# Performance work log

Hardware: AMD Instinct MI355X
Metric: run time of the kernel (lower is better)

Reference implementation:

```python
import jax, jax.numpy as jnp
import numpy as np

N_USERS = 100000
N_TIRES = 100000
N_BRANDS = 100
N_SIZES = 500
HGT = 128
SPEC = 64
TEXT = 384
TPROJ = 64
HID = 128
OUT = 64
T_EVENTS = 2000000


def _lin_init(key, fan_in, fan_out):
    kw, kb = jax.random.split(key)
    s = 1.0 / np.sqrt(fan_in)
    W = jax.random.uniform(kw, (fan_in, fan_out), jnp.float32, -s, s)
    b = jax.random.uniform(kb, (fan_out,), jnp.float32, -s, s)
    return W, b


def setup_inputs() -> dict:
    key = jax.random.key(0)
    ks = jax.random.split(key, 18)
    inp = {
        "h_user": jax.random.normal(ks[0], (N_USERS, HGT), jnp.float32),
        "h_tire": jax.random.normal(ks[1], (N_TIRES, HGT), jnp.float32),
        "h_brand": jax.random.normal(ks[2], (N_BRANDS, HGT), jnp.float32),
        "h_size": jax.random.normal(ks[3], (N_SIZES, HGT), jnp.float32),
        "tire_specs": jax.random.normal(ks[4], (N_TIRES, SPEC), jnp.float32),
        "text_emb": jax.random.normal(ks[5], (N_TIRES, TEXT), jnp.float32),
        "tire_brand_idx": jax.random.randint(ks[6], (N_TIRES,), 0, N_BRANDS, jnp.int32),
        "tire_size_idx": jax.random.randint(ks[7], (N_TIRES,), 0, N_SIZES, jnp.int32),
        "hist_items": jax.random.randint(ks[8], (T_EVENTS,), 0, N_TIRES, jnp.int32),
        "hist_segments": jnp.sort(jax.random.randint(ks[9], (T_EVENTS,), 0, N_USERS, jnp.int32)),
    }
    # text projection
    inp["W_tp"], inp["b_tp"] = _lin_init(ks[10], TEXT, TPROJ)
    # item tower MLP: in = 3*HGT + SPEC + TPROJ = 512
    item_in = 3 * HGT + SPEC + TPROJ
    inp["W_i1"], inp["b_i1"] = _lin_init(ks[11], item_in, HID)
    inp["W_i2"], inp["b_i2"] = _lin_init(ks[12], HID, HID)
    inp["W_i3"], inp["b_i3"] = _lin_init(ks[13], HID, OUT)
    # user tower MLP: in = HGT + OUT = 192
    user_in = HGT + OUT
    inp["W_u1"], inp["b_u1"] = _lin_init(ks[14], user_in, HID)
    inp["W_u2"], inp["b_u2"] = _lin_init(ks[15], HID, HID)
    inp["W_u3"], inp["b_u3"] = _lin_init(ks[16], HID, OUT)
    return inp


def _mlp(x, W1, b1, W2, b2, W3, b3):
    h = jax.nn.relu(x @ W1 + b1)
    h = jax.nn.relu(h @ W2 + b2)
    return h @ W3 + b3


def _l2norm(x):
    n = jnp.sqrt(jnp.sum(x * x, axis=-1, keepdims=True))
    return x / jnp.maximum(n, 1e-12)


def reference(h_user, h_tire, h_brand, h_size, tire_specs, text_emb,
              tire_brand_idx, tire_size_idx, hist_items, hist_segments,
              W_tp, b_tp, W_i1, b_i1, W_i2, b_i2, W_i3, b_i3,
              W_u1, b_u1, W_u2, b_u2, W_u3, b_u3):
    n_users = h_user.shape[0]
    # item tower (dropout = identity in eval)
    text_proj = jax.nn.relu(text_emb @ W_tp + b_tp)  # [T, 64]
    x_item = jnp.concatenate(
        [h_tire, h_brand[tire_brand_idx], h_size[tire_size_idx], tire_specs, text_proj],
        axis=-1)  # [T, 512]
    item_vec = _l2norm(_mlp(x_item, W_i1, b_i1, W_i2, b_i2, W_i3, b_i3))  # [T, 64]
    # ragged history mean-pool as one segment-mean pass
    gathered = item_vec[hist_items]  # [E, 64]
    sums = jax.ops.segment_sum(gathered, hist_segments, num_segments=n_users)
    counts = jax.ops.segment_sum(jnp.ones((hist_items.shape[0],), item_vec.dtype),
                                 hist_segments, num_segments=n_users)[:, None]
    history_pool = jnp.where(counts > 0, sums / jnp.maximum(counts, 1.0), 0.0)
    # user tower
    x_user = jnp.concatenate([h_user, history_pool], axis=-1)  # [U, 192]
    user_vec = _l2norm(_mlp(x_user, W_u1, b_u1, W_u2, b_u2, W_u3, b_u3))  # [U, 64]
    return user_vec, item_vec
```

## Files before the change

### kernel.cpp

```cpp
#include <hip/hip_runtime.h>

typedef __bf16 bf16;
typedef __bf16 bf16x4 __attribute__((ext_vector_type(4)));
typedef __bf16 bf16x8 __attribute__((ext_vector_type(8)));
typedef float f32x4 __attribute__((ext_vector_type(4)));

__device__ inline float bfbits(unsigned u) { return __builtin_bit_cast(float, u); }

__device__ inline bf16x8 cvt8p(f32x4 x0, f32x4 x1) {
  bf16x8 a;
  a[0] = (bf16)x0[0]; a[1] = (bf16)x0[1]; a[2] = (bf16)x0[2]; a[3] = (bf16)x0[3];
  a[4] = (bf16)x1[0]; a[5] = (bf16)x1[1]; a[6] = (bf16)x1[2]; a[7] = (bf16)x1[3];
  return a;
}

#define MFMA16(a, b, c) __builtin_amdgcn_mfma_f32_16x16x32_bf16((a), (b), (c), 0, 0, 0)

__device__ inline void gload16(const void* g, void* l) {
  __builtin_amdgcn_global_load_lds(
      (const __attribute__((address_space(1))) void*)g,
      (__attribute__((address_space(3))) void*)l, 16, 0, 0);
}

#define BARRIER()                      \
  do {                                 \
    asm volatile("" ::: "memory");     \
    __builtin_amdgcn_s_barrier();      \
    asm volatile("" ::: "memory");     \
  } while (0)

template <int N>
__device__ inline void waitcnt_vm() {
  asm volatile("s_waitcnt vmcnt(%0)" ::"i"(N) : "memory");
}

struct WEnt { const float* src; bf16* dst; int K; int N; int mode; int base; };
struct WprepArgs { WEnt e[9]; int nent; int total; float* zb; };

__global__ __launch_bounds__(256) void wprep_all(WprepArgs a) {
  int idx = blockIdx.x * 256 + threadIdx.x;
  if (idx < 128) a.zb[idx] = 0.0f;
  if (idx >= a.total) return;
  int ei = 0;
  while (ei + 1 < a.nent && idx >= a.e[ei + 1].base) ++ei;
  const WEnt E = a.e[ei];
  int li = idx - E.base;
  int lane = li & 63, fi = li >> 6;
  int NT = E.N / 16;
  int kt = fi / NT, nt = fi % NT;
  int krow = kt * 32 + ((lane >> 4) << 3);
  int col = nt * 16 + (lane & 15);
  bf16* d = E.dst + (size_t)li * 8;
#pragma unroll
  for (int j = 0; j < 8; ++j) {
    int r = krow + j;
    if (E.mode == 1) r = (r < 128) ? r : r + 256;
    d[j] = (bf16)E.src[(size_t)r * E.N + col];
  }
}

__global__ __launch_bounds__(256) void seg_bounds(const int* __restrict__ hsegs,
                                                  int* __restrict__ bound, int E, int U) {
  int e = blockIdx.x * 256 + threadIdx.x;
  if (e > E) return;
  if (e == 0) {
    int b = hsegs[0];
    for (int u = 0; u <= b; ++u) bound[u] = 0;
  } else if (e == E) {
    int a = hsegs[E - 1];
    for (int u = a + 1; u <= U; ++u) bound[u] = E;
  } else {
    int a = hsegs[e - 1], b = hsegs[e];
    for (int u = a + 1; u <= b; ++u) bound[u] = e;
  }
}

struct GemmArgs {
  const void* a0; const bf16* wfrag; const float* bias; void* out; int M;
};

template <int K, int N, int NW>
__global__ __launch_bounds__(NW * 64) void gemm_k(GemmArgs g) {
  constexpr int KT = K / 32, NT = N / 16;
  constexpr int TROWS = NW * 32;
  __shared__ bf16 wlds[K * N];
  {
    const uint4* s = (const uint4*)g.wfrag;
    uint4* d = (uint4*)wlds;
    constexpr int CH = K * N * 2 / 16;
    for (int i = threadIdx.x; i < CH; i += NW * 64) d[i] = s[i];
  }
  __syncthreads();

  const int lane = threadIdx.x & 63;
  const int wave = threadIdx.x >> 6;
  const int kgo = (lane >> 4) << 3;
  const int ntiles = (g.M + TROWS - 1) / TROWS;

  for (int tile = blockIdx.x; tile < ntiles; tile += gridDim.x) {
    const int rowbase = tile * TROWS;
    const int rw = rowbase + wave * 16 + (lane & 15);
    const int r0 = min(rw, g.M - 1);
    const int r1 = min(rw + NW * 16, g.M - 1);

    f32x4 acc[2][NT] = {};
#pragma unroll 2
    for (int kt = 0; kt < KT; ++kt) {
      const int kc = kt * 32 + kgo;
      const f32x4* q0 = (const f32x4*)((const float*)g.a0 + (size_t)r0 * K + kc);
      const f32x4* q1 = (const f32x4*)((const float*)g.a0 + (size_t)r1 * K + kc);
      bf16x8 a0 = cvt8p(q0[0], q0[1]);
      bf16x8 a1 = cvt8p(q1[0], q1[1]);
      const bf16x8* bp = ((const bf16x8*)wlds) + kt * NT * 64 + lane;
#pragma unroll
      for (int nt = 0; nt < NT; ++nt) {
        bf16x8 b = bp[nt * 64];
        acc[0][nt] = MFMA16(a0, b, acc[0][nt]);
        acc[1][nt] = MFMA16(a1, b, acc[1][nt]);
      }
    }

    const int colbase = lane & 15;
    const int rgrp = (lane >> 4) * 4;
#pragma unroll
    for (int m = 0; m < 2; ++m) {
      const int rbase = rowbase + m * (NW * 16) + wave * 16 + rgrp;
#pragma unroll
      for (int j = 0; j < 4; ++j) {
        const int r = rbase + j;
        if (r < g.M) {
#pragma unroll
          for (int nt = 0; nt < NT; ++nt) {
            float v = acc[m][nt][j] + g.bias[colbase + nt * 16];
            ((float*)g.out)[(size_t)r * N + colbase + nt * 16] = v;
          }
        }
      }
    }
  }
}

struct TpArgs { const float* text; const bf16* wf; const float* bias; bf16* out; int M; };

__global__ __launch_bounds__(256, 4) void tp_k(TpArgs g) {
  __shared__ float abuf[2][128 * 32];
  const int tid = threadIdx.x, lane = tid & 63, wave = tid >> 6;
  const int kgo = (lane >> 4) << 3, colbase = lane & 15, r4 = (lane >> 4) * 4;
  const int rowbase = blockIdx.x << 7;

  auto stage = [&](int kt, int bi) {
#pragma unroll
    for (int i = 0; i < 4; ++i) {
      const int q = i * 256 + wave * 64 + lane;
      const int row = q >> 3;
      const int c = (lane & 7) ^ (row & 7);
      const int rg = min(rowbase + row, g.M - 1);
      const float* src = g.text + (size_t)rg * 384 + kt * 32 + c * 4;
      gload16(src, (char*)abuf[bi] + (size_t)(i * 256 + wave * 64) * 16);
    }
  };

  stage(0, 0);
  f32x4 acc[2][4] = {};
  for (int kt = 0; kt < 12; ++kt) {
    if (kt + 1 < 12) {
      stage(kt + 1, (kt + 1) & 1);
      waitcnt_vm<4>();
    } else {
      waitcnt_vm<0>();
    }
    BARRIER();
    const float* buf = abuf[kt & 1];
#pragma unroll
    for (int m = 0; m < 2; ++m) {
      const int row = m * 64 + wave * 16 + colbase;
      const int c0 = kgo >> 2;
      f32x4 x0 = *(const f32x4*)(buf + row * 32 + ((c0 ^ (row & 7)) << 2));
      f32x4 x1 = *(const f32x4*)(buf + row * 32 + (((c0 + 1) ^ (row & 7)) << 2));
      bf16x8 a = cvt8p(x0, x1);
      const bf16x8* bp = ((const bf16x8*)g.wf) + kt * 4 * 64 + lane;
#pragma unroll
      for (int nt = 0; nt < 4; ++nt)
        acc[m][nt] = MFMA16(a, bp[nt * 64], acc[m][nt]);
    }
    BARRIER();
  }

#pragma unroll
  for (int m = 0; m < 2; ++m) {
    const int rbase = rowbase + m * 64 + wave * 16 + r4;
#pragma unroll
    for (int j = 0; j < 4; ++j) {
      const int r = rbase + j;
      if (r < g.M) {
#pragma unroll
        for (int nt = 0; nt < 4; ++nt) {
          float v = fmaxf(acc[m][nt][j] + g.bias[colbase + nt * 16], 0.0f);
          g.out[(size_t)r * 64 + colbase + nt * 16] = (bf16)v;
        }
      }
    }
  }
}

struct TowerArgs {
  const void* a0; const void* a1; const void* a2;
  const int* bidx; const int* sidx;
  const float* brandC; const float* sizeC;
  const bf16* wf1; const bf16* wf2; const bf16* wf3;
  const float* b1; const float* b2; const float* b3;
  float* out; bf16* out2; int M;
};

__device__ inline bf16x8 read_afrag(const bf16* hw, int lane, int kt) {
  const int row = lane & 15;
  const int c8 = (kt * 4 + (lane >> 4)) ^ (row & 7);
  return *(const bf16x8*)(hw + row * 128 + c8 * 8);
}

template <int KT1, int DEPTH, int ASRC, int BS>
__global__ __launch_bounds__(512, 2) void tower_p(TowerArgs g) {
  static_assert(KT1 % DEPTH == 0, "pipeline rotation requires DEPTH | KT1");
  constexpr int FK = (ASRC == 2) ? 6 : 4;
  __shared__ bf16 w1[KT1 * 32 * 128];
  __shared__ bf16 w2[128 * 128];
  __shared__ bf16 w3[128 * 64];
  __shared__ bf16 ht[8][16 * 128];
  {
    const int tid = threadIdx.x;
    const uint4* s1 = (const uint4*)g.wf1; uint4* d1 = (uint4*)w1;
    for (int i = tid; i < KT1 * 32 * 128 * 2 / 16; i += 512) d1[i] = s1[i];
    const uint4* s2 = (const uint4*)g.wf2; uint4* d2 = (uint4*)w2;
    for (int i = tid; i < 128 * 128 * 2 / 16; i += 512) d2[i] = s2[i];
    const uint4* s3 = (const uint4*)g.wf3; uint4* d3 = (uint4*)w3;
    for (int i = tid; i < 128 * 64 * 2 / 16; i += 512) d3[i] = s3[i];
  }
  __syncthreads();

  const int lane = threadIdx.x & 63, wave = threadIdx.x >> 6;
  const int kgo = (lane >> 4) << 3, colbase = lane & 15, r4 = (lane >> 4) * 4;
  bf16* hw = ht[wave];
  const int ntiles = (g.M + 255) >> 8;
  const int nb = gridDim.x;

  struct Ptrs { const float* tA; const float* tB; const float* sA; const float* sB;
                const bf16* pA; const bf16* pB; };
  auto mk = [&](int t) {
    Ptrs p;
    const int rA = min(t * 256 + wave * 16 + colbase, g.M - 1);
    const int rB = min(t * 256 + 128 + wave * 16 + colbase, g.M - 1);
    p.tA = (const float*)g.a0 + (size_t)rA * 128;
    p.tB = (const float*)g.a0 + (size_t)rB * 128;
    if constexpr (ASRC == 2) {
      p.sA = (const float*)g.a1 + (size_t)rA * 64;
      p.sB = (const float*)g.a1 + (size_t)rB * 64;
      p.pA = (const bf16*)g.a2 + (size_t)rA * 64;
      p.pB = (const bf16*)g.a2 + (size_t)rB * 64;
    } else {
      p.sA = nullptr; p.sB = nullptr;
      p.pA = (const bf16*)g.a1 + (size_t)rA * 64;
      p.pB = (const bf16*)g.a1 + (size_t)rB * 64;
    }
    return p;
  };

  f32x4 st[DEPTH][4];
  auto issue = [&](f32x4* s, const Ptrs& p, int kt) {
    if (kt < 4) {
      const f32x4* qa = (const f32x4*)(p.tA + kt * 32 + kgo);
      const f32x4* qb = (const f32x4*)(p.tB + kt * 32 + kgo);
      s[0] = qa[0]; s[1] = qa[1]; s[2] = qb[0]; s[3] = qb[1];
    } else if (ASRC == 2 && kt < 6) {
      const f32x4* qa = (const f32x4*)(p.sA + (kt - 4) * 32 + kgo);
      const f32x4* qb = (const f32x4*)(p.sB + (kt - 4) * 32 + kgo);
      s[0] = qa[0]; s[1] = qa[1]; s[2] = qb[0]; s[3] = qb[1];
    } else {
      const int ko = kt - FK;
      s[0] = *(const f32x4*)(p.pA + ko * 32 + kgo);
      s[2] = *(const f32x4*)(p.pB + ko * 32 + kgo);
    }
  };

  int tile = blockIdx.x;
  Ptrs P = mk(tile);
  int tn = tile + nb; if (tn >= ntiles) tn = tile;
  Ptrs Pn = mk(tn);

#pragma unroll
  for (int s = 0; s < DEPTH; ++s) issue(st[s], P, s);

  for (;;) {
    f32x4 acc1[2][8] = {};
#pragma unroll
    for (int kt = 0; kt < KT1; ++kt) {
      const int s = kt % DEPTH;
      bf16x8 a0, a1;
      if (kt < FK) {
        a0 = cvt8p(st[s][0], st[s][1]);
        a1 = cvt8p(st[s][2], st[s][3]);
      } else {
        a0 = __builtin_bit_cast(bf16x8, st[s][0]);
        a1 = __builtin_bit_cast(bf16x8, st[s][2]);
      }
      const bf16x8* bp = ((const bf16x8*)w1) + kt * 8 * 64 + lane;
#pragma unroll
      for (int nt = 0; nt < 8; ++nt) {
        bf16x8 b = bp[nt * 64];
        acc1[0][nt] = MFMA16(a0, b, acc1[0][nt]);
        acc1[1][nt] = MFMA16(a1, b, acc1[1][nt]);
      }
      if (kt + DEPTH < KT1) issue(st[s], P, kt + DEPTH);
      else issue(st[s], Pn, kt + DEPTH - KT1);
    }

    const int rowbase = tile * 256;
    f32x4 acc3[2][4] = {};
#pragma unroll
    for (int m = 0; m < 2; ++m) {
      const int rbase = rowbase + m * 128 + wave * 16 + r4;
#pragma unroll
      for (int j = 0; j < 4; ++j) {
        const int row = r4 + j;
        const float* bc = nullptr; const float* sc = nullptr;
        if constexpr (BS != 0) {
          const int rr = min(rbase + j, g.M - 1);
          bc = g.brandC + (size_t)g.bidx[rr] * 128;
          sc = g.sizeC + (size_t)g.sidx[rr] * 128;
        }
#pragma unroll
        for (int nt = 0; nt < 8; ++nt) {
          const int col = colbase + nt * 16;
          float v = acc1[m][nt][j];
          if constexpr (BS != 0) v += bc[col] + sc[col];
          else v += g.b1[col];
          const int c8 = (col >> 3) ^ (row & 7);
          hw[row * 128 + c8 * 8 + (col & 7)] = (bf16)fmaxf(v, 0.0f);
        }
      }
      f32x4 acc2[8] = {};
#pragma unroll
      for (int kt = 0; kt < 4; ++kt) {
        bf16x8 af = read_afrag(hw, lane, kt);
        const bf16x8* bp = ((const bf16x8*)w2) + kt * 8 * 64 + lane;
#pragma unroll
        for (int nt = 0; nt < 8; ++nt)
          acc2[nt] = MFMA16(af, bp[nt * 64], acc2[nt]);
      }
#pragma unroll
      for (int j = 0; j < 4; ++j) {
        const int row = r4 + j;
#pragma unroll
        for (int nt = 0; nt < 8; ++nt) {
          const int col = colbase + nt * 16;
          float v = fmaxf(acc2[nt][j] + g.b2[col], 0.0f);
          const int c8 = (col >> 3) ^ (row & 7);
          hw[row * 128 + c8 * 8 + (col & 7)] = (bf16)v;
        }
      }
#pragma unroll
      for (int kt = 0; kt < 4; ++kt) {
        bf16x8 af = read_afrag(hw, lane, kt);
        const bf16x8* bq = ((const bf16x8*)w3) + kt * 4 * 64 + lane;
#pragma unroll
        for (int nt = 0; nt < 4; ++nt)
          acc3[m][nt] = MFMA16(af, bq[nt * 64], acc3[m][nt]);
      }
    }

#pragma unroll
    for (int m = 0; m < 2; ++m) {
      const int rbase = rowbase + m * 128 + wave * 16 + r4;
#pragma unroll
      for (int j = 0; j < 4; ++j) {
        float vv[4];
        float ssq = 0.0f;
#pragma unroll
        for (int nt = 0; nt < 4; ++nt) {
          float v = acc3[m][nt][j] + g.b3[colbase + nt * 16];
          vv[nt] = v;
          ssq += v * v;
        }
        ssq += __shfl_xor(ssq, 1);
        ssq += __shfl_xor(ssq, 2);
        ssq += __shfl_xor(ssq, 4);
        ssq += __shfl_xor(ssq, 8);
        const float scale = 1.0f / fmaxf(sqrtf(ssq), 1e-12f);
        const int r = rbase + j;
        if (r < g.M) {
          float* o = g.out + (size_t)r * 64 + colbase;
#pragma unroll
          for (int nt = 0; nt < 4; ++nt) o[nt * 16] = vv[nt] * scale;
          if (g.out2) {
            bf16* o2 = g.out2 + (size_t)r * 64 + colbase;
#pragma unroll
            for (int nt = 0; nt < 4; ++nt) o2[nt * 16] = (bf16)(vv[nt] * scale);
          }
        }
      }
    }

    if (tn == tile) break;
    tile = tn; P = Pn;
    tn = tile + nb; if (tn >= ntiles) tn = tile;
    Pn = mk(tn);
  }
}

__global__ __launch_bounds__(256) void pool_k(const int* __restrict__ hitems,
                                              const int* __restrict__ bound,
                                              const bf16* __restrict__ itemb,
                                              bf16* __restrict__ pool, int U) {
  const int lane = threadIdx.x & 63;
  const int wid = blockIdx.x * 4 + (threadIdx.x >> 6);
  const int stride = gridDim.x * 4;
  const int grp = lane >> 4, li = lane & 15;
  for (int u = wid; u < U; u += stride) {
    const int s = bound[u], e = bound[u + 1];
    f32x4 s0 = {0.f, 0.f, 0.f, 0.f}, s1 = {0.f, 0.f, 0.f, 0.f};
    f32x4 s2 = {0.f, 0.f, 0.f, 0.f}, s3 = {0.f, 0.f, 0.f, 0.f};
    int i = s + grp;
    for (; i + 12 < e; i += 16) {
      int a0 = hitems[i], a1 = hitems[i + 4], a2 = hitems[i + 8], a3 = hitems[i + 12];
      uint2 r0 = *(const uint2*)(itemb + (size_t)a0 * 64 + li * 4);
      uint2 r1 = *(const uint2*)(itemb + (size_t)a1 * 64 + li * 4);
      uint2 r2 = *(const uint2*)(itemb + (size_t)a2 * 64 + li * 4);
      uint2 r3 = *(const uint2*)(itemb + (size_t)a3 * 64 + li * 4);
      s0[0] += bfbits(r0.x << 16); s0[1] += bfbits(r0.x & 0xffff0000u);
      s0[2] += bfbits(r0.y << 16); s0[3] += bfbits(r0.y & 0xffff0000u);
      s1[0] += bfbits(r1.x << 16); s1[1] += bfbits(r1.x & 0xffff0000u);
      s1[2] += bfbits(r1.y << 16); s1[3] += bfbits(r1.y & 0xffff0000u);
      s2[0] += bfbits(r2.x << 16); s2[1] += bfbits(r2.x & 0xffff0000u);
      s2[2] += bfbits(r2.y << 16); s2[3] += bfbits(r2.y & 0xffff0000u);
      s3[0] += bfbits(r3.x << 16); s3[1] += bfbits(r3.x & 0xffff0000u);
      s3[2] += bfbits(r3.y << 16); s3[3] += bfbits(r3.y & 0xffff0000u);
    }
    for (; i < e; i += 4) {
      int a0 = hitems[i];
      uint2 r0 = *(const uint2*)(itemb + (size_t)a0 * 64 + li * 4);
      s0[0] += bfbits(r0.x << 16); s0[1] += bfbits(r0.x & 0xffff0000u);
      s0[2] += bfbits(r0.y << 16); s0[3] += bfbits(r0.y & 0xffff0000u);
    }
#pragma unroll
    for (int c = 0; c < 4; ++c) s0[c] += s1[c] + s2[c] + s3[c];
#pragma unroll
    for (int c = 0; c < 4; ++c) {
      s0[c] += __shfl_xor(s0[c], 16);
      s0[c] += __shfl_xor(s0[c], 32);
    }
    const int cnt = e - s;
    const float inv = (cnt > 0) ? 1.0f / (float)cnt : 0.0f;
    if (grp == 0) {
      bf16x4 o;
      o[0] = (bf16)(s0[0] * inv); o[1] = (bf16)(s0[1] * inv);
      o[2] = (bf16)(s0[2] * inv); o[3] = (bf16)(s0[3] * inv);
      *(bf16x4*)(pool + (size_t)u * 64 + li * 4) = o;
    }
  }
}

extern "C" void kernel_launch(void* const* d_in, const int* in_sizes, int n_in,
                              void* d_out, int out_size, void* d_ws, size_t ws_size,
                              hipStream_t stream) {
  const float* h_user = (const float*)d_in[0];
  const float* h_tire = (const float*)d_in[1];
  const float* h_brand = (const float*)d_in[2];
  const float* h_size = (const float*)d_in[3];
  const float* specs = (const float*)d_in[4];
  const float* text = (const float*)d_in[5];
  const int* bidx = (const int*)d_in[6];
  const int* sidx = (const int*)d_in[7];
  const int* hitems = (const int*)d_in[8];
  const int* hsegs = (const int*)d_in[9];
  const float* W_tp = (const float*)d_in[10]; const float* b_tp = (const float*)d_in[11];
  const float* W_i1 = (const float*)d_in[12]; const float* b_i1 = (const float*)d_in[13];
  const float* W_i2 = (const float*)d_in[14]; const float* b_i2 = (const float*)d_in[15];
  const float* W_i3 = (const float*)d_in[16]; const float* b_i3 = (const float*)d_in[17];
  const float* W_u1 = (const float*)d_in[18]; const float* b_u1 = (const float*)d_in[19];
  const float* W_u2 = (const float*)d_in[20]; const float* b_u2 = (const float*)d_in[21];
  const float* W_u3 = (const float*)d_in[22]; const float* b_u3 = (const float*)d_in[23];

  const int U = in_sizes[0] / 128;
  const int T = in_sizes[4] / 64;
  const int E = in_sizes[8];

  char* ws = (char*)d_ws;
  size_t off = 0;
  auto alloc = [&](size_t bytes) -> char* {
    char* p = ws + off;
    off += (bytes + 255) & ~(size_t)255;
    return p;
  };
  bf16* wf_tp  = (bf16*)alloc(384 * 64 * 2);
  bf16* wf_i1a = (bf16*)alloc(256 * 128 * 2);
  bf16* wf_ib  = (bf16*)alloc(128 * 128 * 2);
  bf16* wf_is  = (bf16*)alloc(128 * 128 * 2);
  bf16* wf_i2  = (bf16*)alloc(128 * 128 * 2);
  bf16* wf_i3  = (bf16*)alloc(128 * 64 * 2);
  bf16* wf_u1  = (bf16*)alloc(192 * 128 * 2);
  bf16* wf_u2  = (bf16*)alloc(128 * 128 * 2);
  bf16* wf_u3  = (bf16*)alloc(128 * 64 * 2);
  float* zb    = (float*)alloc(128 * 4);
  float* brandC = (float*)alloc(100 * 128 * 4);
  float* sizeC  = (float*)alloc(500 * 128 * 4);
  bf16* tpbuf = (bf16*)alloc((size_t)T * 64 * 2);
  bf16* pool  = (bf16*)alloc((size_t)U * 64 * 2);
  bf16* itemb = (bf16*)alloc((size_t)T * 64 * 2);
  int* bound  = (int*)alloc((size_t)(U + 1) * 4);
  (void)ws_size; (void)n_in; (void)out_size;

  WprepArgs wa = {};
  auto addent = [&](int i, const float* src, bf16* dst, int K, int N, int mode, int& run) {
    wa.e[i] = {src, dst, K, N, mode, run};
    run += (K / 32) * (N / 16) * 64;
  };
  int run = 0;
  addent(0, W_tp, wf_tp, 384, 64, 0, run);
  addent(1, W_i1, wf_i1a, 256, 128, 1, run);
  addent(2, W_i1 + 128 * 128, wf_ib, 128, 128, 0, run);
  addent(3, W_i1 + 256 * 128, wf_is, 128, 128, 0, run);
  addent(4, W_i2, wf_i2, 128, 128, 0, run);
  addent(5, W_i3, wf_i3, 128, 64, 0, run);
  addent(6, W_u1, wf_u1, 192, 128, 0, run);
  addent(7, W_u2, wf_u2, 128, 128, 0, run);
  addent(8, W_u3, wf_u3, 128, 64, 0, run);
  wa.nent = 9; wa.total = run; wa.zb = zb;
  wprep_all<<<(run + 255) / 256, 256, 0, stream>>>(wa);

  seg_bounds<<<(E + 256) / 256, 256, 0, stream>>>(hsegs, bound, E, U);

  {
    GemmArgs a = {}; a.a0 = h_brand; a.wfrag = wf_ib; a.bias = b_i1; a.out = brandC; a.M = 100;
    gemm_k<128, 128, 4><<<1, 256, 0, stream>>>(a);
  }
  {
    GemmArgs a = {}; a.a0 = h_size; a.wfrag = wf_is; a.bias = zb; a.out = sizeC; a.M = 500;
    gemm_k<128, 128, 4><<<4, 256, 0, stream>>>(a);
  }
  {
    TpArgs a = {text, wf_tp, b_tp, tpbuf, T};
    tp_k<<<(T + 127) / 128, 256, 0, stream>>>(a);
  }

  float* out_user = (float*)d_out;
  float* out_item = out_user + (size_t)U * 64;

  {
    TowerArgs a = {};
    a.a0 = h_tire; a.a1 = specs; a.a2 = tpbuf;
    a.bidx = bidx; a.sidx = sidx; a.brandC = brandC; a.sizeC = sizeC;
    a.wf1 = wf_i1a; a.wf2 = wf_i2; a.wf3 = wf_i3;
    a.b1 = zb; a.b2 = b_i2; a.b3 = b_i3;
    a.out = out_item; a.out2 = itemb; a.M = T;
    const int nt = (T + 255) / 256;
    tower_p<8, 4, 2, 1><<<min(256, nt), 512, 0, stream>>>(a);
  }

  pool_k<<<(U + 3) / 4, 256, 0, stream>>>(hitems, bound, itemb, pool, U);

  {
    TowerArgs a = {};
    a.a0 = h_user; a.a1 = pool;
    a.wf1 = wf_u1; a.wf2 = wf_u2; a.wf3 = wf_u3;
    a.b1 = b_u1; a.b2 = b_u2; a.b3 = b_u3;
    a.out = out_user; a.out2 = nullptr; a.M = U;
    const int nt = (U + 255) / 256;
    tower_p<6, 2, 3, 0><<<min(256, nt), 512, 0, stream>>>(a);
  }
}
```

Measured before the change: 246.7 us.

## Replace register-pipelined persistent tower kernel with simple one-tile-per-block loop

Removes the manual multi-stage register prefetch pipeline and the persistent grid capped at 256 blocks from the tower kernels. Each block now handles one 256-row tile with direct loads inside the K loop. The aim is lower register pressure and more blocks in flight, letting the hardware hide latency. This gives up the explicit overlap of the next tile's loads with current compute.

```diff
diff --git a/kernel.cpp b/kernel.cpp
--- a/kernel.cpp
+++ b/kernel.cpp
@@ -12,6 +12,10 @@
   a[0] = (bf16)x0[0]; a[1] = (bf16)x0[1]; a[2] = (bf16)x0[2]; a[3] = (bf16)x0[3];
   a[4] = (bf16)x1[0]; a[5] = (bf16)x1[1]; a[6] = (bf16)x1[2]; a[7] = (bf16)x1[3];
   return a;
+}
+__device__ inline bf16x8 cvt8(const float* p) {
+  const f32x4* q = (const f32x4*)p;
+  return cvt8p(q[0], q[1]);
 }
 
 #define MFMA16(a, b, c) __builtin_amdgcn_mfma_f32_16x16x32_bf16((a), (b), (c), 0, 0, 0)
@@ -107,10 +111,8 @@
 #pragma unroll 2
     for (int kt = 0; kt < KT; ++kt) {
       const int kc = kt * 32 + kgo;
-      const f32x4* q0 = (const f32x4*)((const float*)g.a0 + (size_t)r0 * K + kc);
-      const f32x4* q1 = (const f32x4*)((const float*)g.a0 + (size_t)r1 * K + kc);
-      bf16x8 a0 = cvt8p(q0[0], q0[1]);
-      bf16x8 a1 = cvt8p(q1[0], q1[1]);
+      bf16x8 a0 = cvt8((const float*)g.a0 + (size_t)r0 * K + kc);
+      bf16x8 a1 = cvt8((const float*)g.a0 + (size_t)r1 * K + kc);
       const bf16x8* bp = ((const bf16x8*)wlds) + kt * NT * 64 + lane;
 #pragma unroll
       for (int nt = 0; nt < NT; ++nt) {
@@ -212,24 +214,38 @@
   float* out; bf16* out2; int M;
 };
 
+template <int ASRC>
+__device__ inline bf16x8 tower_load_a(const TowerArgs& g, int r, int kc) {
+  if constexpr (ASRC == 2) {
+    if (kc < 128) return cvt8((const float*)g.a0 + (size_t)r * 128 + kc);
+    else if (kc < 192) return cvt8((const float*)g.a1 + (size_t)r * 64 + (kc - 128));
+    else return *(const bf16x8*)((const bf16*)g.a2 + (size_t)r * 64 + (kc - 192));
+  } else {
+    if (kc < 128) return cvt8((const float*)g.a0 + (size_t)r * 128 + kc);
+    else return *(const bf16x8*)((const bf16*)g.a1 + (size_t)r * 64 + (kc - 128));
+  }
+}
+
 __device__ inline bf16x8 read_afrag(const bf16* hw, int lane, int kt) {
   const int row = lane & 15;
   const int c8 = (kt * 4 + (lane >> 4)) ^ (row & 7);
   return *(const bf16x8*)(hw + row * 128 + c8 * 8);
 }
 
-template <int KT1, int DEPTH, int ASRC, int BS>
-__global__ __launch_bounds__(512, 2) void tower_p(TowerArgs g) {
-  static_assert(KT1 % DEPTH == 0, "pipeline rotation requires DEPTH | KT1");
-  constexpr int FK = (ASRC == 2) ? 6 : 4;
-  __shared__ bf16 w1[KT1 * 32 * 128];
-  __shared__ bf16 w2[128 * 128];
-  __shared__ bf16 w3[128 * 64];
-  __shared__ bf16 ht[8][16 * 128];
+template <int K1, int ASRC, int BS>
+__global__ __launch_bounds__(512, 2) void tower_k(TowerArgs g) {
+  constexpr int KT1 = K1 / 32;
+  constexpr int NW = 8;
+  constexpr int TROWS = NW * 32;
+  __shared__ bf16 lds[K1 * 128 + 128 * 128 + 128 * 64 + NW * 16 * 128];
+  bf16* w1 = lds;
+  bf16* w2 = lds + K1 * 128;
+  bf16* w3 = w2 + 128 * 128;
+  bf16* ht = w3 + 128 * 64;
   {
     const int tid = threadIdx.x;
     const uint4* s1 = (const uint4*)g.wf1; uint4* d1 = (uint4*)w1;
-    for (int i = tid; i < KT1 * 32 * 128 * 2 / 16; i += 512) d1[i] = s1[i];
+    for (int i = tid; i < K1 * 128 * 2 / 16; i += 512) d1[i] = s1[i];
     const uint4* s2 = (const uint4*)g.wf2; uint4* d2 = (uint4*)w2;
     for (int i = tid; i < 128 * 128 * 2 / 16; i += 512) d2[i] = s2[i];
     const uint4* s3 = (const uint4*)g.wf3; uint4* d3 = (uint4*)w3;
@@ -237,71 +253,26 @@
   }
   __syncthreads();
 
-  const int lane = threadIdx.x & 63, wave = threadIdx.x >> 6;
-  const int kgo = (lane >> 4) << 3, colbase = lane & 15, r4 = (lane >> 4) * 4;
-  bf16* hw = ht[wave];
-  const int ntiles = (g.M + 255) >> 8;
-  const int nb = gridDim.x;
-
-  struct Ptrs { const float* tA; const float* tB; const float* sA; const float* sB;
-                const bf16* pA; const bf16* pB; };
-  auto mk = [&](int t) {
-    Ptrs p;
-    const int rA = min(t * 256 + wave * 16 + colbase, g.M - 1);
-    const int rB = min(t * 256 + 128 + wave * 16 + colbase, g.M - 1);
-    p.tA = (const float*)g.a0 + (size_t)rA * 128;
-    p.tB = (const float*)g.a0 + (size_t)rB * 128;
-    if constexpr (ASRC == 2) {
-      p.sA = (const float*)g.a1 + (size_t)rA * 64;
-      p.sB = (const float*)g.a1 + (size_t)rB * 64;
-      p.pA = (const bf16*)g.a2 + (size_t)rA * 64;
-      p.pB = (const bf16*)g.a2 + (size_t)rB * 64;
-    } else {
-      p.sA = nullptr; p.sB = nullptr;
-      p.pA = (const bf16*)g.a1 + (size_t)rA * 64;
-      p.pB = (const bf16*)g.a1 + (size_t)rB * 64;
-    }
-    return p;
-  };
-
-  f32x4 st[DEPTH][4];
-  auto issue = [&](f32x4* s, const Ptrs& p, int kt) {
-    if (kt < 4) {
-      const f32x4* qa = (const f32x4*)(p.tA + kt * 32 + kgo);
-      const f32x4* qb = (const f32x4*)(p.tB + kt * 32 + kgo);
-      s[0] = qa[0]; s[1] = qa[1]; s[2] = qb[0]; s[3] = qb[1];
-    } else if (ASRC == 2 && kt < 6) {
-      const f32x4* qa = (const f32x4*)(p.sA + (kt - 4) * 32 + kgo);
-      const f32x4* qb = (const f32x4*)(p.sB + (kt - 4) * 32 + kgo);
-      s[0] = qa[0]; s[1] = qa[1]; s[2] = qb[0]; s[3] = qb[1];
-    } else {
-      const int ko = kt - FK;
-      s[0] = *(const f32x4*)(p.pA + ko * 32 + kgo);
-      s[2] = *(const f32x4*)(p.pB + ko * 32 + kgo);
-    }
-  };
-
-  int tile = blockIdx.x;
-  Ptrs P = mk(tile);
-  int tn = tile + nb; if (tn >= ntiles) tn = tile;
-  Ptrs Pn = mk(tn);
-
-#pragma unroll
-  for (int s = 0; s < DEPTH; ++s) issue(st[s], P, s);
-
-  for (;;) {
+  const int lane = threadIdx.x & 63;
+  const int wave = threadIdx.x >> 6;
+  const int kgo = (lane >> 4) << 3;
+  const int colbase = lane & 15;
+  const int r4 = (lane >> 4) * 4;
+  bf16* hw = ht + wave * (16 * 128);
+  const int ntiles = (g.M + TROWS - 1) / TROWS;
+
+  for (int tile = blockIdx.x; tile < ntiles; tile += gridDim.x) {
+    const int rowbase = tile * TROWS;
+    const int rw = rowbase + wave * 16 + colbase;
+    const int r0 = min(rw, g.M - 1);
+    const int r1 = min(rw + NW * 16, g.M - 1);
+
     f32x4 acc1[2][8] = {};
-#pragma unroll
+#pragma unroll 2
     for (int kt = 0; kt < KT1; ++kt) {
-      const int s = kt % DEPTH;
-      bf16x8 a0, a1;
-      if (kt < FK) {
-        a0 = cvt8p(st[s][0], st[s][1]);
-        a1 = cvt8p(st[s][2], st[s][3]);
-      } else {
-        a0 = __builtin_bit_cast(bf16x8, st[s][0]);
-        a1 = __builtin_bit_cast(bf16x8, st[s][2]);
-      }
+      const int kc = kt * 32 + kgo;
+      bf16x8 a0 = tower_load_a<ASRC>(g, r0, kc);
+      bf16x8 a1 = tower_load_a<ASRC>(g, r1, kc);
       const bf16x8* bp = ((const bf16x8*)w1) + kt * 8 * 64 + lane;
 #pragma unroll
       for (int nt = 0; nt < 8; ++nt) {
@@ -309,15 +280,12 @@
         acc1[0][nt] = MFMA16(a0, b, acc1[0][nt]);
         acc1[1][nt] = MFMA16(a1, b, acc1[1][nt]);
       }
-      if (kt + DEPTH < KT1) issue(st[s], P, kt + DEPTH);
-      else issue(st[s], Pn, kt + DEPTH - KT1);
-    }
-
-    const int rowbase = tile * 256;
+    }
+
     f32x4 acc3[2][4] = {};
 #pragma unroll
     for (int m = 0; m < 2; ++m) {
-      const int rbase = rowbase + m * 128 + wave * 16 + r4;
+      const int rbase = rowbase + m * (NW * 16) + wave * 16 + r4;
 #pragma unroll
       for (int j = 0; j < 4; ++j) {
         const int row = r4 + j;
@@ -333,18 +301,19 @@
           float v = acc1[m][nt][j];
           if constexpr (BS != 0) v += bc[col] + sc[col];
           else v += g.b1[col];
+          v = fmaxf(v, 0.0f);
           const int c8 = (col >> 3) ^ (row & 7);
-          hw[row * 128 + c8 * 8 + (col & 7)] = (bf16)fmaxf(v, 0.0f);
+          hw[row * 128 + c8 * 8 + (col & 7)] = (bf16)v;
         }
       }
       f32x4 acc2[8] = {};
 #pragma unroll
       for (int kt = 0; kt < 4; ++kt) {
-        bf16x8 af = read_afrag(hw, lane, kt);
+        bf16x8 a = read_afrag(hw, lane, kt);
         const bf16x8* bp = ((const bf16x8*)w2) + kt * 8 * 64 + lane;
 #pragma unroll
         for (int nt = 0; nt < 8; ++nt)
-          acc2[nt] = MFMA16(af, bp[nt * 64], acc2[nt]);
+          acc2[nt] = MFMA16(a, bp[nt * 64], acc2[nt]);
       }
 #pragma unroll
       for (int j = 0; j < 4; ++j) {
@@ -359,17 +328,17 @@
       }
 #pragma unroll
       for (int kt = 0; kt < 4; ++kt) {
-        bf16x8 af = read_afrag(hw, lane, kt);
-        const bf16x8* bq = ((const bf16x8*)w3) + kt * 4 * 64 + lane;
+        bf16x8 a = read_afrag(hw, lane, kt);
+        const bf16x8* bp = ((const bf16x8*)w3) + kt * 4 * 64 + lane;
 #pragma unroll
         for (int nt = 0; nt < 4; ++nt)
-          acc3[m][nt] = MFMA16(af, bq[nt * 64], acc3[m][nt]);
+          acc3[m][nt] = MFMA16(a, bp[nt * 64], acc3[m][nt]);
       }
     }
 
 #pragma unroll
     for (int m = 0; m < 2; ++m) {
-      const int rbase = rowbase + m * 128 + wave * 16 + r4;
+      const int rbase = rowbase + m * (NW * 16) + wave * 16 + r4;
 #pragma unroll
       for (int j = 0; j < 4; ++j) {
         float vv[4];
@@ -398,11 +367,6 @@
         }
       }
     }
-
-    if (tn == tile) break;
-    tile = tn; P = Pn;
-    tn = tile + nb; if (tn >= ntiles) tn = tile;
-    Pn = mk(tn);
   }
 }
 
@@ -551,8 +515,7 @@
     a.wf1 = wf_i1a; a.wf2 = wf_i2; a.wf3 = wf_i3;
     a.b1 = zb; a.b2 = b_i2; a.b3 = b_i3;
     a.out = out_item; a.out2 = itemb; a.M = T;
-    const int nt = (T + 255) / 256;
-    tower_p<8, 4, 2, 1><<<min(256, nt), 512, 0, stream>>>(a);
+    tower_k<256, 2, 1><<<(T + 255) / 256, 512, 0, stream>>>(a);
   }
 
   pool_k<<<(U + 3) / 4, 256, 0, stream>>>(hitems, bound, itemb, pool, U);
@@ -563,7 +526,6 @@
     a.wf1 = wf_u1; a.wf2 = wf_u2; a.wf3 = wf_u3;
     a.b1 = b_u1; a.b2 = b_u2; a.b3 = b_u3;
     a.out = out_user; a.out2 = nullptr; a.M = U;
-    const int nt = (U + 255) / 256;
-    tower_p<6, 2, 3, 0><<<min(256, nt), 512, 0, stream>>>(a);
-  }
-}
+    tower_k<192, 3, 0><<<(U + 255) / 256, 512, 0, stream>>>(a);
+  }
+}
```

Measured after the change: 235.9 us. 1.05x faster.
